# Optimization experiments

Hardware: AMD Instinct MI355X
Metric: run time of the kernel (lower is better)

The kernel has to match this reference:

```python
import jax, jax.numpy as jnp
import numpy as np

TAU = 0.1
EPS_NORM = 1e-12  # torch F.normalize clamp
EPS_DEN = 1e-6


def setup_inputs() -> dict:
    key = jax.random.key(0)
    k1, k2, k3, k4 = jax.random.split(key, 4)
    B, C, H, W = 4, 128, 64, 64
    feat_A = jax.random.normal(k1, (B, C, H, W), dtype=jnp.float32)
    feat_B = jax.random.normal(k2, (B, C, H, W), dtype=jnp.float32)
    H_mat = jax.random.normal(k3, (B, 3, 3), dtype=jnp.float32)
    valid_mask = jax.random.uniform(k4, (B, H, W), dtype=jnp.float32)
    return {"feat_A": feat_A, "feat_B": feat_B, "H_mat": H_mat, "valid_mask": valid_mask}


def _l2_normalize(x, axis):
    n = jnp.sqrt(jnp.sum(x * x, axis=axis, keepdims=True))
    return x / jnp.maximum(n, EPS_NORM)


def reference(feat_A, feat_B, H_mat, valid_mask):
    B, C, H, W = feat_A.shape
    HW = H * W
    fA = _l2_normalize(feat_A.reshape(B, C, HW), axis=1)  # [B, C, HW]
    fB = _l2_normalize(feat_B.reshape(B, C, HW), axis=1)  # [B, C, HW]
    # sim[b, n, m] = <fA[:, :, n], fB[:, :, m]> / tau
    sim = jnp.einsum('bcn,bcm->bnm', fA, fB) / TAU  # [B, HW, HW]
    # torch CE with input [B, HW, HW], labels arange(HW): class axis is 1,
    # so logits for position k are the column sim[b, :, k], target = k.
    lse = jax.nn.logsumexp(sim, axis=1)               # [B, HW] (over class axis)
    diag = jnp.einsum('bkk->bk', sim)                 # sim[b, k, k]
    loss = lse - diag                                  # [B, HW], per-position CE
    mask_flat = valid_mask.reshape(B, HW)
    return (loss * mask_flat).sum() / (mask_flat.sum() + EPS_DEN)
```

## Files before the change

### kernel.cpp

```cpp
#include <hip/hip_runtime.h>
#include <math.h>

#define BB 4
#define CC 128
#define HW 4096
#define SCF 3.798282565f

typedef short short8 __attribute__((ext_vector_type(8)));
typedef float f32x4 __attribute__((ext_vector_type(4)));

static __device__ inline unsigned short f2bf(float f) {
  unsigned int u = __float_as_uint(f);
  u += 0x7fffu + ((u >> 16) & 1u);
  return (unsigned short)(u >> 16);
}

static __device__ inline float fast_exp2(float x) {
#if __has_builtin(__builtin_amdgcn_exp2f)
  return __builtin_amdgcn_exp2f(x);
#else
  return exp2f(x);
#endif
}

__global__ __launch_bounds__(256) void k_prep(const float* __restrict__ fA,
                                              const float* __restrict__ fB,
                                              unsigned short* __restrict__ fAn,
                                              unsigned short* __restrict__ fBn,
                                              float* __restrict__ diag,
                                              float* __restrict__ expsum,
                                              float* __restrict__ acc) {
  __shared__ float sA[32 * 129];
  __shared__ float sB[32 * 129];
  __shared__ float red[3 * 256];

  const int bid = blockIdx.x;
  const int b   = bid >> 7;
  const int n0  = (bid & 127) * 32;
  const int tid = threadIdx.x;
  const int cR  = tid >> 5;
  const int n   = tid & 31;

  if (bid == 0 && tid == 0) { acc[0] = 0.f; acc[1] = 0.f; ((unsigned*)acc)[2] = 0u; }

  const float* pa = fA + (size_t)b * CC * HW + n0 + n;
  const float* pb = fB + (size_t)b * CC * HW + n0 + n;

  float ssa = 0.f, ssb = 0.f, dot = 0.f;
  #pragma unroll
  for (int it = 0; it < 16; ++it) {
    int c = it * 8 + cR;
    float va = pa[(size_t)c * HW];
    float vb = pb[(size_t)c * HW];
    sA[n * 129 + c] = va;
    sB[n * 129 + c] = vb;
    ssa = fmaf(va, va, ssa);
    ssb = fmaf(vb, vb, ssb);
    dot = fmaf(va, vb, dot);
  }
  red[tid] = ssa; red[256 + tid] = ssb; red[512 + tid] = dot;
  __syncthreads();

  if (tid < 32) {
    float sa = 0.f, sb = 0.f, dt = 0.f;
    #pragma unroll
    for (int k = 0; k < 8; ++k) {
      sa += red[k * 32 + tid];
      sb += red[256 + k * 32 + tid];
      dt += red[512 + k * 32 + tid];
    }
    float ia = 1.f / fmaxf(sqrtf(sa), 1e-12f);
    float ib = 1.f / fmaxf(sqrtf(sb), 1e-12f);
    int gidx = b * HW + n0 + tid;
    diag[gidx]   = dt * ia * ib * 10.f;
    expsum[gidx] = 0.f;
    red[tid]      = ia * SCF;
    red[32 + tid] = ib * SCF;
  }
  __syncthreads();

  #pragma unroll
  for (int r = 0; r < 2; ++r) {
    int L  = r * 256 + tid;
    int nn = L >> 4;
    int q  = L & 15;
    int c0 = (q ^ (nn & 7)) * 8;
    size_t base = ((size_t)b * HW + n0 + nn) * 128 + q * 8;
    {
      float sc = red[nn];
      const float* s = &sA[nn * 129 + c0];
      uint4 v;
      v.x = f2bf(s[0]*sc) | ((unsigned)f2bf(s[1]*sc) << 16);
      v.y = f2bf(s[2]*sc) | ((unsigned)f2bf(s[3]*sc) << 16);
      v.z = f2bf(s[4]*sc) | ((unsigned)f2bf(s[5]*sc) << 16);
      v.w = f2bf(s[6]*sc) | ((unsigned)f2bf(s[7]*sc) << 16);
      *(uint4*)(fAn + base) = v;
    }
    {
      float sc = red[32 + nn];
      const float* s = &sB[nn * 129 + c0];
      uint4 v;
      v.x = f2bf(s[0]*sc) | ((unsigned)f2bf(s[1]*sc) << 16);
      v.y = f2bf(s[2]*sc) | ((unsigned)f2bf(s[3]*sc) << 16);
      v.z = f2bf(s[4]*sc) | ((unsigned)f2bf(s[5]*sc) << 16);
      v.w = f2bf(s[6]*sc) | ((unsigned)f2bf(s[7]*sc) << 16);
      *(uint4*)(fBn + base) = v;
    }
  }
}

__global__ __launch_bounds__(256, 2) void k_main(const unsigned short* __restrict__ fAn,
                                                 const unsigned short* __restrict__ fBn,
                                                 float* __restrict__ expsum) {
  __shared__ unsigned short sB[128 * 128];
  __shared__ unsigned short sA[128 * 128];

  const int bid = blockIdx.x;
  const int x   = bid & 7;
  const int t   = bid >> 3;
  const int b   = x & 3;
  const int nq  = (x >> 2) | ((t & 1) << 1);
  const int mt  = t >> 1;
  const int m0  = mt * 128;
  const int nbase = nq * 1024;
  const int tid = threadIdx.x;

  const unsigned short* gB = fBn + ((size_t)b * HW + m0) * 128;
  #pragma unroll
  for (int r = 0; r < 8; ++r) {
    int L = r * 256 + tid;
    __builtin_amdgcn_global_load_lds(
        (const __attribute__((address_space(1))) unsigned int*)(gB + (size_t)L * 8),
        (__attribute__((address_space(3))) unsigned int*)(sB + L * 8), 16, 0, 0);
  }

  const int wv   = tid >> 6;
  const int lane = tid & 63;
  const int ml   = lane & 15;
  const int g    = lane >> 4;
  const int wn   = (wv & 1) * 64;
  const int wm   = (wv >> 1) * 64;

  float colAcc[4] = {0.f, 0.f, 0.f, 0.f};

  for (int it = 0; it < 8; ++it) {
    __syncthreads();
    const unsigned short* gA = fAn + ((size_t)b * HW + nbase + it * 128) * 128;
    #pragma unroll
    for (int r = 0; r < 8; ++r) {
      int L = r * 256 + tid;
      __builtin_amdgcn_global_load_lds(
          (const __attribute__((address_space(1))) unsigned int*)(gA + (size_t)L * 8),
          (__attribute__((address_space(3))) unsigned int*)(sA + L * 8), 16, 0, 0);
    }
    __syncthreads();

    f32x4 acc[4][4] = {};
    #pragma unroll
    for (int kc = 0; kc < 4; ++kc) {
      short8 af[4], bf[4];
      int q = kc * 4 + g;
      #pragma unroll
      for (int s = 0; s < 4; ++s) {
        int na = wn + s * 16 + ml;
        af[s] = *(const short8*)(sA + na * 128 + ((q ^ (na & 7)) * 8));
        int nb = wm + s * 16 + ml;
        bf[s] = *(const short8*)(sB + nb * 128 + ((q ^ (nb & 7)) * 8));
      }
      #pragma unroll
      for (int i = 0; i < 4; ++i)
        #pragma unroll
        for (int j = 0; j < 4; ++j)
          acc[i][j] = __builtin_amdgcn_mfma_f32_16x16x32_bf16(af[i], bf[j], acc[i][j], 0, 0, 0);
    }
    #pragma unroll
    for (int j = 0; j < 4; ++j) {
      float e = 0.f;
      #pragma unroll
      for (int i = 0; i < 4; ++i)
        #pragma unroll
        for (int r = 0; r < 4; ++r)
          e += fast_exp2(acc[i][j][r]);
      colAcc[j] += e;
    }
  }

  #pragma unroll
  for (int j = 0; j < 4; ++j) {
    float e = colAcc[j];
    e += __shfl_xor(e, 16, 64);
    e += __shfl_xor(e, 32, 64);
    if (lane < 16)
      atomicAdd(&expsum[(size_t)b * HW + m0 + wm + j * 16 + lane], e);
  }
}

__global__ __launch_bounds__(256) void k_loss(const float* __restrict__ diag,
                                              const float* __restrict__ expsum,
                                              const float* __restrict__ mask,
                                              float* __restrict__ acc,
                                              float* __restrict__ out) {
  __shared__ float rn[4], rd[4];
  const int i = blockIdx.x * 256 + threadIdx.x;
  float lse = __logf(expsum[i]);
  float mv  = mask[i];
  float num = mv * (lse - diag[i]);
  #pragma unroll
  for (int off = 32; off; off >>= 1) {
    num += __shfl_down(num, off, 64);
    mv  += __shfl_down(mv,  off, 64);
  }
  const int lane = threadIdx.x & 63, wv = threadIdx.x >> 6;
  if (lane == 0) { rn[wv] = num; rd[wv] = mv; }
  __syncthreads();
  if (threadIdx.x == 0) {
    float n = rn[0] + rn[1] + rn[2] + rn[3];
    float d = rd[0] + rd[1] + rd[2] + rd[3];
    atomicAdd(&acc[0], n);
    atomicAdd(&acc[1], d);
    __threadfence();
    unsigned prev = atomicAdd((unsigned*)(acc + 2), 1u);
    if (prev == 63u) {
      float fn = atomicAdd(&acc[0], 0.f);
      float fd = atomicAdd(&acc[1], 0.f);
      out[0] = fn / (fd + 1e-6f);
    }
  }
}

extern "C" void kernel_launch(void* const* d_in, const int* in_sizes, int n_in,
                              void* d_out, int out_size, void* d_ws, size_t ws_size,
                              hipStream_t stream) {
  const float* feat_A = (const float*)d_in[0];
  const float* feat_B = (const float*)d_in[1];
  const float* vmask  = (const float*)d_in[3];

  unsigned short* fAn = (unsigned short*)d_ws;
  unsigned short* fBn = fAn + (size_t)BB * HW * CC;
  float* diag   = (float*)(fBn + (size_t)BB * HW * CC);
  float* expsum = diag + BB * HW;
  float* acc    = expsum + BB * HW;
  float* out    = (float*)d_out;

  k_prep<<<512, 256, 0, stream>>>(feat_A, feat_B, fAn, fBn, diag, expsum, acc);
  k_main<<<512, 256, 0, stream>>>(fAn, fBn, expsum);
  k_loss<<<64,  256, 0, stream>>>(diag, expsum, vmask, acc, out);
}
```

Before: 96.60 us.

## Double-buffer A tiles with register-resident B fragments and fuse loss into main

Restructures the main similarity kernel to keep the B fragments in registers for the whole block, double-buffer the A tiles in LDS so the next tile's global-to-LDS load overlaps the current MFMA and exp work, and drop one barrier per iteration. The separate loss kernel is removed: the last block to finish, found through an atomic counter, computes the masked log-sum-exp reduction and writes the output, which saves one launch. The risks are much higher register pressure from holding 32 short8 fragments per thread, which may hurt occupancy at two blocks per SM, and a serial tail where a single block reduces all 16K positions. The exp builtin is also swapped for exp2f.

```diff
diff --git a/kernel.cpp b/kernel.cpp
--- a/kernel.cpp
+++ b/kernel.cpp
@@ -13,14 +13,6 @@
   unsigned int u = __float_as_uint(f);
   u += 0x7fffu + ((u >> 16) & 1u);
   return (unsigned short)(u >> 16);
-}
-
-static __device__ inline float fast_exp2(float x) {
-#if __has_builtin(__builtin_amdgcn_exp2f)
-  return __builtin_amdgcn_exp2f(x);
-#else
-  return exp2f(x);
-#endif
 }
 
 __global__ __launch_bounds__(256) void k_prep(const float* __restrict__ fA,
@@ -111,9 +103,15 @@
 
 __global__ __launch_bounds__(256, 2) void k_main(const unsigned short* __restrict__ fAn,
                                                  const unsigned short* __restrict__ fBn,
-                                                 float* __restrict__ expsum) {
-  __shared__ unsigned short sB[128 * 128];
-  __shared__ unsigned short sA[128 * 128];
+                                                 float* __restrict__ expsum,
+                                                 const float* __restrict__ diag,
+                                                 const float* __restrict__ mask,
+                                                 float* __restrict__ acc,
+                                                 float* __restrict__ out) {
+  __shared__ unsigned short lds[2 * 16384];
+  unsigned short* buf0 = lds;
+  unsigned short* buf1 = lds + 16384;
+  __shared__ bool lastFlag;
 
   const int bid = blockIdx.x;
   const int x   = bid & 7;
@@ -125,15 +123,6 @@
   const int nbase = nq * 1024;
   const int tid = threadIdx.x;
 
-  const unsigned short* gB = fBn + ((size_t)b * HW + m0) * 128;
-  #pragma unroll
-  for (int r = 0; r < 8; ++r) {
-    int L = r * 256 + tid;
-    __builtin_amdgcn_global_load_lds(
-        (const __attribute__((address_space(1))) unsigned int*)(gB + (size_t)L * 8),
-        (__attribute__((address_space(3))) unsigned int*)(sB + L * 8), 16, 0, 0);
-  }
-
   const int wv   = tid >> 6;
   const int lane = tid & 63;
   const int ml   = lane & 15;
@@ -141,38 +130,50 @@
   const int wn   = (wv & 1) * 64;
   const int wm   = (wv >> 1) * 64;
 
-  float colAcc[4] = {0.f, 0.f, 0.f, 0.f};
-
-  for (int it = 0; it < 8; ++it) {
-    __syncthreads();
-    const unsigned short* gA = fAn + ((size_t)b * HW + nbase + it * 128) * 128;
+  auto stage = [&](const unsigned short* gsrc, unsigned short* dst) {
     #pragma unroll
     for (int r = 0; r < 8; ++r) {
       int L = r * 256 + tid;
       __builtin_amdgcn_global_load_lds(
-          (const __attribute__((address_space(1))) unsigned int*)(gA + (size_t)L * 8),
-          (__attribute__((address_space(3))) unsigned int*)(sA + L * 8), 16, 0, 0);
-    }
-    __syncthreads();
-
-    f32x4 acc[4][4] = {};
-    #pragma unroll
-    for (int kc = 0; kc < 4; ++kc) {
-      short8 af[4], bf[4];
-      int q = kc * 4 + g;
-      #pragma unroll
-      for (int s = 0; s < 4; ++s) {
-        int na = wn + s * 16 + ml;
-        af[s] = *(const short8*)(sA + na * 128 + ((q ^ (na & 7)) * 8));
-        int nb = wm + s * 16 + ml;
-        bf[s] = *(const short8*)(sB + nb * 128 + ((q ^ (nb & 7)) * 8));
-      }
+          (const __attribute__((address_space(1))) unsigned int*)(gsrc + (size_t)L * 8),
+          (__attribute__((address_space(3))) unsigned int*)(dst + L * 8), 16, 0, 0);
+    }
+  };
+  const unsigned short* gAbase = fAn + ((size_t)b * HW + nbase) * 128;
+
+  stage(fBn + ((size_t)b * HW + m0) * 128, buf1);
+  stage(gAbase, buf0);
+  __syncthreads();
+
+  short8 bf[4][4], af[4][4];
+  #pragma unroll
+  for (int kc = 0; kc < 4; ++kc) {
+    int q = kc * 4 + g;
+    #pragma unroll
+    for (int j = 0; j < 4; ++j) {
+      int nb = wm + j * 16 + ml;
+      bf[kc][j] = *(const short8*)(buf1 + nb * 128 + ((q ^ (nb & 7)) * 8));
+    }
+    #pragma unroll
+    for (int i = 0; i < 4; ++i) {
+      int na = wn + i * 16 + ml;
+      af[kc][i] = *(const short8*)(buf0 + na * 128 + ((q ^ (na & 7)) * 8));
+    }
+  }
+  __syncthreads();
+  stage(gAbase + (size_t)1 * 16384, buf1);
+
+  float colAcc[4] = {0.f, 0.f, 0.f, 0.f};
+
+  for (int it = 0; it < 8; ++it) {
+    f32x4 acc4[4][4] = {};
+    #pragma unroll
+    for (int kc = 0; kc < 4; ++kc)
       #pragma unroll
       for (int i = 0; i < 4; ++i)
         #pragma unroll
         for (int j = 0; j < 4; ++j)
-          acc[i][j] = __builtin_amdgcn_mfma_f32_16x16x32_bf16(af[i], bf[j], acc[i][j], 0, 0, 0);
-    }
+          acc4[i][j] = __builtin_amdgcn_mfma_f32_16x16x32_bf16(af[kc][i], bf[kc][j], acc4[i][j], 0, 0, 0);
     #pragma unroll
     for (int j = 0; j < 4; ++j) {
       float e = 0.f;
@@ -180,9 +181,23 @@
       for (int i = 0; i < 4; ++i)
         #pragma unroll
         for (int r = 0; r < 4; ++r)
-          e += fast_exp2(acc[i][j][r]);
+          e += exp2f(acc4[i][j][r]);
       colAcc[j] += e;
     }
+    if (it == 7) break;
+    __syncthreads();
+    const unsigned short* bufc = (it & 1) ? buf0 : buf1;
+    #pragma unroll
+    for (int kc = 0; kc < 4; ++kc) {
+      int q = kc * 4 + g;
+      #pragma unroll
+      for (int i = 0; i < 4; ++i) {
+        int na = wn + i * 16 + ml;
+        af[kc][i] = *(const short8*)(bufc + na * 128 + ((q ^ (na & 7)) * 8));
+      }
+    }
+    if (it < 6)
+      stage(gAbase + (size_t)(it + 2) * 16384, (it & 1) ? buf1 : buf0);
   }
 
   #pragma unroll
@@ -193,37 +208,34 @@
     if (lane < 16)
       atomicAdd(&expsum[(size_t)b * HW + m0 + wm + j * 16 + lane], e);
   }
-}
-
-__global__ __launch_bounds__(256) void k_loss(const float* __restrict__ diag,
-                                              const float* __restrict__ expsum,
-                                              const float* __restrict__ mask,
-                                              float* __restrict__ acc,
-                                              float* __restrict__ out) {
-  __shared__ float rn[4], rd[4];
-  const int i = blockIdx.x * 256 + threadIdx.x;
-  float lse = __logf(expsum[i]);
-  float mv  = mask[i];
-  float num = mv * (lse - diag[i]);
-  #pragma unroll
-  for (int off = 32; off; off >>= 1) {
-    num += __shfl_down(num, off, 64);
-    mv  += __shfl_down(mv,  off, 64);
-  }
-  const int lane = threadIdx.x & 63, wv = threadIdx.x >> 6;
-  if (lane == 0) { rn[wv] = num; rd[wv] = mv; }
-  __syncthreads();
-  if (threadIdx.x == 0) {
-    float n = rn[0] + rn[1] + rn[2] + rn[3];
-    float d = rd[0] + rd[1] + rd[2] + rd[3];
-    atomicAdd(&acc[0], n);
-    atomicAdd(&acc[1], d);
+
+  __syncthreads();
+  if (tid == 0) {
     __threadfence();
-    unsigned prev = atomicAdd((unsigned*)(acc + 2), 1u);
-    if (prev == 63u) {
-      float fn = atomicAdd(&acc[0], 0.f);
-      float fd = atomicAdd(&acc[1], 0.f);
-      out[0] = fn / (fd + 1e-6f);
+    lastFlag = (atomicAdd((unsigned*)(acc + 2), 1u) == 511u);
+  }
+  __syncthreads();
+  if (lastFlag) {
+    float num = 0.f, den = 0.f;
+    #pragma unroll 4
+    for (int i = tid; i < BB * HW; i += 256) {
+      float es = __hip_atomic_load(expsum + i, __ATOMIC_RELAXED, __HIP_MEMORY_SCOPE_AGENT);
+      float mv = mask[i];
+      num = fmaf(mv, __logf(es) - diag[i], num);
+      den += mv;
+    }
+    #pragma unroll
+    for (int off = 32; off; off >>= 1) {
+      num += __shfl_down(num, off, 64);
+      den += __shfl_down(den, off, 64);
+    }
+    float* red = (float*)lds;
+    if (lane == 0) { red[wv] = num; red[8 + wv] = den; }
+    __syncthreads();
+    if (tid == 0) {
+      float n = red[0] + red[1] + red[2] + red[3];
+      float d = red[8] + red[9] + red[10] + red[11];
+      out[0] = n / (d + 1e-6f);
     }
   }
 }
@@ -243,6 +255,5 @@
   float* out    = (float*)d_out;
 
   k_prep<<<512, 256, 0, stream>>>(feat_A, feat_B, fAn, fBn, diag, expsum, acc);
-  k_main<<<512, 256, 0, stream>>>(fAn, fBn, expsum);
-  k_loss<<<64,  256, 0, stream>>>(diag, expsum, vmask, acc, out);
-}
+  k_main<<<512, 256, 0, stream>>>(fAn, fBn, expsum, diag, vmask, acc, out);
+}
```

Result: slower. 113.0 us (+17.0%).
